# Optimization experiments

Hardware: AMD Instinct MI355X
Metric: run time of the kernel (lower is better)

Reference implementation:

```python
import jax, jax.numpy as jnp
from jax import lax
import numpy as np

NUM_BINS = 16
EPS = 1e-8


def setup_inputs() -> dict:
    key = jax.random.key(0)
    x = jax.random.normal(key, (32, 512, 4096), dtype=jnp.float32)
    return {"x": x}


def reference(x):
    B, C, L = x.shape  # [B, C, L]
    nb = NUM_BINS
    # g = mean over sequence -> [B, C]
    g = x.mean(axis=2)
    # cosine similarity along channel dim between each column x[:, :, l] and g
    dot = jnp.einsum('bcl,bc->bl', x, g)                      # [B, L]
    xn = jnp.sqrt(jnp.sum(x * x, axis=1))                     # [B, L]
    gn = jnp.sqrt(jnp.sum(g * g, axis=1, keepdims=True))      # [B, 1]
    cos = dot / jnp.maximum(xn * gn, EPS)                     # [B, L]
    S = cos.reshape(-1)                                       # [B*L]
    # torch.linspace on tensor endpoints detaches -> stop_gradient for fidelity
    min_S = lax.stop_gradient(S.min())
    max_S = lax.stop_gradient(S.max())
    levels = min_S + jnp.arange(nb, dtype=S.dtype) * (max_S - min_S) / (nb - 1)  # [nb]
    # soft triangular binning: (1 - |S - L_n|) inside a half-width 0.5/nb window
    d = jnp.abs(S[:, None] - levels[None, :])                 # [B*L, nb]
    E = jnp.where(d < 0.5 / nb, 1.0 - d, 0.0)
    E = E.reshape(B, L, nb)
    count_map = E.sum(axis=1)                                 # [B, nb]
    count_map = count_map / count_map.sum(axis=1, keepdims=True)
    # adaptive_avg_pool1d from length 1 to C//nb just replicates the value
    out = jnp.broadcast_to(count_map[:, :, None], (B, nb, C // nb))
    return out
```

## Files before the change

kernel.cpp:

```cpp
#include <hip/hip_runtime.h>

typedef float f4 __attribute__((ext_vector_type(4)));

#define BB 32
#define CC 512
#define LL 4096
#define NB 16
#define EPSF 1e-8f

__global__ __launch_bounds__(256, 2)
void k_main(const float* __restrict__ x, float* __restrict__ g,
            f4* __restrict__ pd4, f4* __restrict__ ps4) {
    __shared__ f4 ldsD[1024], ldsS[1024];
    const int tid = threadIdx.x;
    const int w = tid >> 6, lane = tid & 63;
    const int b  = blockIdx.x >> 4;
    const int c0 = (blockIdx.x & 15) * 32;

    f4 dA[16], sA[16];
#pragma unroll
    for (int i = 0; i < 16; ++i) { dA[i] = (f4)0.f; sA[i] = (f4)0.f; }

    const f4* base = (const f4*)(x + ((size_t)b * CC + c0 + w * 8) * LL);
    for (int cc = 0; cc < 8; ++cc) {
        const f4* row = base + (size_t)cc * 1024;
        f4 v[16];
#pragma unroll
        for (int i = 0; i < 16; ++i) v[i] = __builtin_nontemporal_load(&row[i * 64 + lane]);
        float s = 0.f;
#pragma unroll
        for (int i = 0; i < 16; ++i) s += (v[i][0] + v[i][1]) + (v[i][2] + v[i][3]);
#pragma unroll
        for (int off = 32; off; off >>= 1) s += __shfl_down(s, off, 64);
        s = __shfl(s, 0, 64);
        const float gv = s * (1.0f / LL);
        if (lane == 0) g[b * CC + c0 + w * 8 + cc] = gv;
#pragma unroll
        for (int i = 0; i < 16; ++i) {
#pragma unroll
            for (int k = 0; k < 4; ++k) {
                dA[i][k] = fmaf(v[i][k], gv, dA[i][k]);
                sA[i][k] = fmaf(v[i][k], v[i][k], sA[i][k]);
            }
        }
    }
    for (int ww = 0; ww < 4; ++ww) {
        if (w == ww) {
#pragma unroll
            for (int i = 0; i < 16; ++i) {
                const int idx = i * 64 + lane;
                if (ww == 0) { ldsD[idx] = dA[i];  ldsS[idx] = sA[i]; }
                else         { ldsD[idx] += dA[i]; ldsS[idx] += sA[i]; }
            }
        }
        __syncthreads();
    }
#pragma unroll
    for (int j = 0; j < 4; ++j) {
        pd4[(size_t)blockIdx.x * 1024 + j * 256 + tid] = ldsD[j * 256 + tid];
        ps4[(size_t)blockIdx.x * 1024 + j * 256 + tid] = ldsS[j * 256 + tid];
    }
}

__global__ void k_reduce(const float* __restrict__ g,
                         const f4* __restrict__ pd4, const f4* __restrict__ ps4,
                         f4* __restrict__ cosv4,
                         float* __restrict__ pmin, float* __restrict__ pmax) {
    const int tid = threadIdx.x;
    const int w = tid >> 6, lane = tid & 63;
    const int b = blockIdx.x >> 3;
    const int q = blockIdx.x & 7;
    const int s = q * 128 + tid;

    f4 g4 = ((const f4*)g)[b * 128 + tid];
    float sq = fmaf(g4[0], g4[0], fmaf(g4[1], g4[1], fmaf(g4[2], g4[2], g4[3] * g4[3])));
#pragma unroll
    for (int off = 32; off; off >>= 1) sq += __shfl_down(sq, off, 64);
    __shared__ float sw[2];
    if (lane == 0) sw[w] = sq;
    __syncthreads();
    const float gn = sqrtf(sw[0] + sw[1]);

    f4 pdv = (f4)0.f, psv = (f4)0.f;
#pragma unroll
    for (int ch = 0; ch < 16; ++ch) {
        pdv += pd4[(((size_t)b * 16 + ch) << 10) + s];
        psv += ps4[(((size_t)b * 16 + ch) << 10) + s];
    }
    f4 cs;
#pragma unroll
    for (int k = 0; k < 4; ++k)
        cs[k] = pdv[k] / fmaxf(sqrtf(psv[k]) * gn, EPSF);
    cosv4[(size_t)b * 1024 + s] = cs;

    float mn = fminf(fminf(cs[0], cs[1]), fminf(cs[2], cs[3]));
    float mx = fmaxf(fmaxf(cs[0], cs[1]), fmaxf(cs[2], cs[3]));
#pragma unroll
    for (int off = 32; off; off >>= 1) {
        mn = fminf(mn, __shfl_down(mn, off, 64));
        mx = fmaxf(mx, __shfl_down(mx, off, 64));
    }
    __shared__ float smn[2], smx[2];
    if (lane == 0) { smn[w] = mn; smx[w] = mx; }
    __syncthreads();
    if (tid == 0) {
        pmin[blockIdx.x] = fminf(smn[0], smn[1]);
        pmax[blockIdx.x] = fmaxf(smx[0], smx[1]);
    }
}

__global__ void k_hist(const float* __restrict__ cosv,
                       const float* __restrict__ pmin, const float* __restrict__ pmax,
                       float* __restrict__ out) {
    const int b = blockIdx.x;
    const int wave = threadIdx.x >> 6, lane = threadIdx.x & 63;

    float mn = pmin[threadIdx.x];
    float mx = pmax[threadIdx.x];
#pragma unroll
    for (int off = 32; off; off >>= 1) {
        mn = fminf(mn, __shfl_down(mn, off, 64));
        mx = fmaxf(mx, __shfl_down(mx, off, 64));
    }
    __shared__ float smn[4], smx[4];
    if (lane == 0) { smn[wave] = mn; smx[wave] = mx; }
    __syncthreads();
    mn = fminf(fminf(smn[0], smn[1]), fminf(smn[2], smn[3]));
    mx = fmaxf(fmaxf(smx[0], smx[1]), fmaxf(smx[2], smx[3]));
    const float range = mx - mn;

    float bins[NB];
#pragma unroll
    for (int n = 0; n < NB; ++n) bins[n] = 0.f;

    const float* cb = cosv + (b << 12);
    for (int l = threadIdx.x; l < LL; l += 256) {
        float s = cb[l];
#pragma unroll
        for (int n = 0; n < NB; ++n) {
            float lev = mn + ((float)n * range) / 15.0f;
            float d = fabsf(s - lev);
            bins[n] += (d < 0.03125f) ? (1.0f - d) : 0.f;
        }
    }
#pragma unroll
    for (int n = 0; n < NB; ++n) {
#pragma unroll
        for (int off = 32; off; off >>= 1) bins[n] += __shfl_down(bins[n], off, 64);
    }
    __shared__ float sb[4][NB];
    if (lane == 0) {
#pragma unroll
        for (int n = 0; n < NB; ++n) sb[wave][n] = bins[n];
    }
    __syncthreads();
    __shared__ float colsum[NB];
    if (threadIdx.x < NB) {
        const int n = threadIdx.x;
        colsum[n] = sb[0][n] + sb[1][n] + sb[2][n] + sb[3][n];
    }
    __syncthreads();
    float total = 0.f;
#pragma unroll
    for (int n = 0; n < NB; ++n) total += colsum[n];
    {
        const int i0 = threadIdx.x;
        out[b * (NB * 32) + i0]       = colsum[i0 >> 5] / total;
        out[b * (NB * 32) + i0 + 256] = colsum[(i0 + 256) >> 5] / total;
    }
}

extern "C" void kernel_launch(void* const* d_in, const int* in_sizes, int n_in,
                              void* d_out, int out_size, void* d_ws, size_t ws_size,
                              hipStream_t stream) {
    const float* x = (const float*)d_in[0];
    float* out = (float*)d_out;
    float* ws  = (float*)d_ws;

    float* g    = ws;
    float* cosv = ws + 16384;
    float* pmin = ws + 16384 + 131072;
    float* pmax = pmin + 256;
    f4*    pd4  = (f4*)(pmax + 256);
    f4*    ps4  = pd4 + 524288;

    k_main<<<512, 256, 0, stream>>>(x, g, pd4, ps4);
    k_reduce<<<256, 128, 0, stream>>>(g, pd4, ps4, (f4*)cosv, pmin, pmax);
    k_hist<<<32, 256, 0, stream>>>(cosv, pmin, pmax, out);
}
```

Before: 69.50 us.

## Split partial-sum reduction across more blocks and drop nontemporal loads

The reduce kernel now runs 512 blocks of 256 threads instead of 256 blocks of 128. Each wave sums 4 of the 16 channel-chunk partials, and the waves combine their results through LDS, so more loads are in flight at once. The min/max partial arrays grow to 512 entries, and the histogram kernel reads two partials per thread. Separately, the main kernel's loads switch from nontemporal to normal cached loads. That could change cache behaviour on the large streaming read of x, in either direction.

```diff
diff --git a/kernel.cpp b/kernel.cpp
--- a/kernel.cpp
+++ b/kernel.cpp
@@ -26,7 +26,7 @@
         const f4* row = base + (size_t)cc * 1024;
         f4 v[16];
 #pragma unroll
-        for (int i = 0; i < 16; ++i) v[i] = __builtin_nontemporal_load(&row[i * 64 + lane]);
+        for (int i = 0; i < 16; ++i) v[i] = row[i * 64 + lane];
         float s = 0.f;
 #pragma unroll
         for (int i = 0; i < 16; ++i) s += (v[i][0] + v[i][1]) + (v[i][2] + v[i][3]);
@@ -62,50 +62,55 @@
     }
 }
 
-__global__ void k_reduce(const float* __restrict__ g,
-                         const f4* __restrict__ pd4, const f4* __restrict__ ps4,
-                         f4* __restrict__ cosv4,
-                         float* __restrict__ pmin, float* __restrict__ pmax) {
+__global__ __launch_bounds__(256, 8)
+void k_reduce(const float* __restrict__ g,
+              const f4* __restrict__ pd4, const f4* __restrict__ ps4,
+              f4* __restrict__ cosv4,
+              float* __restrict__ pmin, float* __restrict__ pmax) {
     const int tid = threadIdx.x;
     const int w = tid >> 6, lane = tid & 63;
-    const int b = blockIdx.x >> 3;
-    const int q = blockIdx.x & 7;
-    const int s = q * 128 + tid;
+    const int b = blockIdx.x >> 4;
+    const int sl = (blockIdx.x & 15) * 64 + lane;
 
-    f4 g4 = ((const f4*)g)[b * 128 + tid];
-    float sq = fmaf(g4[0], g4[0], fmaf(g4[1], g4[1], fmaf(g4[2], g4[2], g4[3] * g4[3])));
+    f4 pdv = (f4)0.f, psv = (f4)0.f;
+    const size_t cb = (size_t)b * 16;
+#pragma unroll
+    for (int c = 0; c < 4; ++c) {
+        const int ch = 4 * w + c;
+        pdv += pd4[((cb + ch) << 10) + sl];
+        psv += ps4[((cb + ch) << 10) + sl];
+    }
+    __shared__ f4 sD[4][64], sS[4][64];
+    sD[w][lane] = pdv;
+    sS[w][lane] = psv;
+
+    const f4* g4p = (const f4*)(g + b * CC);
+    f4 ga = g4p[lane], gb2 = g4p[64 + lane];
+    float sq = 0.f;
+#pragma unroll
+    for (int k = 0; k < 4; ++k) sq = fmaf(ga[k], ga[k], fmaf(gb2[k], gb2[k], sq));
 #pragma unroll
     for (int off = 32; off; off >>= 1) sq += __shfl_down(sq, off, 64);
-    __shared__ float sw[2];
-    if (lane == 0) sw[w] = sq;
+    const float gn = sqrtf(__shfl(sq, 0, 64));
+
     __syncthreads();
-    const float gn = sqrtf(sw[0] + sw[1]);
+    if (tid < 64) {
+        f4 d = ((sD[0][lane] + sD[1][lane]) + sD[2][lane]) + sD[3][lane];
+        f4 ssum = ((sS[0][lane] + sS[1][lane]) + sS[2][lane]) + sS[3][lane];
+        f4 cs;
+#pragma unroll
+        for (int k = 0; k < 4; ++k)
+            cs[k] = d[k] / fmaxf(sqrtf(ssum[k]) * gn, EPSF);
+        cosv4[(size_t)b * 1024 + sl] = cs;
 
-    f4 pdv = (f4)0.f, psv = (f4)0.f;
+        float mn = fminf(fminf(cs[0], cs[1]), fminf(cs[2], cs[3]));
+        float mx = fmaxf(fmaxf(cs[0], cs[1]), fmaxf(cs[2], cs[3]));
 #pragma unroll
-    for (int ch = 0; ch < 16; ++ch) {
-        pdv += pd4[(((size_t)b * 16 + ch) << 10) + s];
-        psv += ps4[(((size_t)b * 16 + ch) << 10) + s];
-    }
-    f4 cs;
-#pragma unroll
-    for (int k = 0; k < 4; ++k)
-        cs[k] = pdv[k] / fmaxf(sqrtf(psv[k]) * gn, EPSF);
-    cosv4[(size_t)b * 1024 + s] = cs;
-
-    float mn = fminf(fminf(cs[0], cs[1]), fminf(cs[2], cs[3]));
-    float mx = fmaxf(fmaxf(cs[0], cs[1]), fmaxf(cs[2], cs[3]));
-#pragma unroll
-    for (int off = 32; off; off >>= 1) {
-        mn = fminf(mn, __shfl_down(mn, off, 64));
-        mx = fmaxf(mx, __shfl_down(mx, off, 64));
-    }
-    __shared__ float smn[2], smx[2];
-    if (lane == 0) { smn[w] = mn; smx[w] = mx; }
-    __syncthreads();
-    if (tid == 0) {
-        pmin[blockIdx.x] = fminf(smn[0], smn[1]);
-        pmax[blockIdx.x] = fmaxf(smx[0], smx[1]);
+        for (int off = 32; off; off >>= 1) {
+            mn = fminf(mn, __shfl_down(mn, off, 64));
+            mx = fmaxf(mx, __shfl_down(mx, off, 64));
+        }
+        if (lane == 0) { pmin[blockIdx.x] = mn; pmax[blockIdx.x] = mx; }
     }
 }
 
@@ -115,8 +120,8 @@
     const int b = blockIdx.x;
     const int wave = threadIdx.x >> 6, lane = threadIdx.x & 63;
 
-    float mn = pmin[threadIdx.x];
-    float mx = pmax[threadIdx.x];
+    float mn = fminf(pmin[threadIdx.x], pmin[threadIdx.x + 256]);
+    float mx = fmaxf(pmax[threadIdx.x], pmax[threadIdx.x + 256]);
 #pragma unroll
     for (int off = 32; off; off >>= 1) {
         mn = fminf(mn, __shfl_down(mn, off, 64));
@@ -180,11 +185,11 @@
     float* g    = ws;
     float* cosv = ws + 16384;
     float* pmin = ws + 16384 + 131072;
-    float* pmax = pmin + 256;
-    f4*    pd4  = (f4*)(pmax + 256);
+    float* pmax = pmin + 512;
+    f4*    pd4  = (f4*)(pmax + 512);
     f4*    ps4  = pd4 + 524288;
 
     k_main<<<512, 256, 0, stream>>>(x, g, pd4, ps4);
-    k_reduce<<<256, 128, 0, stream>>>(g, pd4, ps4, (f4*)cosv, pmin, pmax);
+    k_reduce<<<512, 256, 0, stream>>>(g, pd4, ps4, (f4*)cosv, pmin, pmax);
     k_hist<<<32, 256, 0, stream>>>(cosv, pmin, pmax, out);
 }
```

New measurement: 66.09 us. 4.9% less time.
